# Performance work log

Measured on AMD Instinct MI355X. Metric: run time of the kernel, lower is better.

The kernel has to match this reference:

```python
import jax, jax.numpy as jnp
import numpy as np

N, T, C, H, W = 4, 8, 512, 14, 14
HEADS = 8
D = C // HEADS            # 64 per-head dim
S = T * H * W             # 1568 sequence length
EPS = 1e-8
NEG = -2.0**32 + 1.0      # padding value used by the original module


def setup_inputs() -> dict:
    key = jax.random.key(0)
    ks = jax.random.split(key, 8)
    shp = (N, T, C, H, W)
    scale = 1.0 / np.sqrt(C)
    return {
        "queries": jax.random.normal(ks[0], shp, jnp.float32),
        "keys": jax.random.normal(ks[1], shp, jnp.float32),
        "values": jax.random.normal(ks[2], shp, jnp.float32),
        "Wq": jax.random.normal(ks[3], (C, C), jnp.float32) * scale,
        "bq": jnp.zeros((C,), jnp.float32),
        "Wk": jax.random.normal(ks[4], (C, C), jnp.float32) * scale,
        "bk": jnp.zeros((C,), jnp.float32),
        "Wv": jax.random.normal(ks[5], (C, C), jnp.float32) * scale,
        "bv": jnp.zeros((C,), jnp.float32),
        "gamma": jnp.ones((C,), jnp.float32),
        "beta": jnp.zeros((C,), jnp.float32),
    }


def _proj(x, Wt, b):
    # 1x1 Conv2d + ReLU over channel dim of (N, T, C, H, W)
    y = jnp.einsum('ntchw,oc->ntohw', x, Wt) + b[None, None, :, None, None]
    return jax.nn.relu(y)


def _flatten(x):
    # (N, T, C, H, W) -> (N, T*H*W, C)
    return x.transpose(0, 1, 3, 4, 2).reshape(N, S, C)


def _split_heads(x):
    # torch.cat(torch.chunk(x, HEADS, dim=2), dim=0): (N, S, C) -> (HEADS*N, S, D)
    return x.reshape(N, S, HEADS, D).transpose(2, 0, 1, 3).reshape(HEADS * N, S, D)


def reference(queries, keys, values, Wq, bq, Wk, bk, Wv, bv, gamma, beta):
    Qf = _flatten(_proj(queries, Wq, bq))
    Kf = _flatten(_proj(keys, Wk, bk))
    Vf = _flatten(_proj(values, Wv, bv))
    q_flat = _flatten(queries)   # residual + query mask source
    k_flat = _flatten(keys)      # key mask source

    Q_ = _split_heads(Qf)
    K_ = _split_heads(Kf)
    V_ = _split_heads(Vf)

    scores = jnp.einsum('bqd,bkd->bqk', Q_, K_) / jnp.sqrt(jnp.float32(D))

    # key padding mask: sign(|sum over C|), tiled over heads -> (HEADS*N, 1, S)
    key_mask = jnp.sign(jnp.abs(k_flat.sum(-1)))          # (N, S)
    km = jnp.tile(key_mask, (HEADS, 1))[:, None, :]
    scores = jnp.where(km == 0.0, NEG, scores)

    attn = jax.nn.softmax(scores, axis=-1)

    # query padding mask (multiplicative) -> (HEADS*N, S, 1)
    query_mask = jnp.sign(jnp.abs(q_flat.sum(-1)))        # (N, S)
    qm = jnp.tile(query_mask, (HEADS, 1))[:, :, None]
    attn = attn * qm

    out = jnp.einsum('bqk,bkd->bqd', attn, V_)
    # merge heads back: inverse of _split_heads
    out = out.reshape(HEADS, N, S, D).transpose(1, 2, 0, 3).reshape(N, S, C)

    out = out + q_flat  # residual

    # custom LayerNorm: torch .std() is unbiased (ddof=1)
    mean = out.mean(-1, keepdims=True)
    std = jnp.sqrt(out.var(-1, ddof=1, keepdims=True))
    out = gamma * (out - mean) / (std + EPS) + beta

    # reshape back to (N, T, C, H, W)
    return out.reshape(N, T, H, W, C).transpose(0, 1, 4, 2, 3)
```

## Files before the change

### kernel.cpp

```cpp
#include <hip/hip_runtime.h>
#include <math.h>

#define N_ 4
#define T_ 8
#define C_ 512
#define H_ 14
#define W_ 14
#define HEADS_ 8
#define D_ 64
#define HW_ 196
#define S_ 1568
#define P_TOT 6272
#define NEGL_ (-1.0e38f)
#define EPS_ 1e-8f
#define QSC_ 0.18033688011112042f

typedef __attribute__((ext_vector_type(8))) short short8v;
typedef __attribute__((ext_vector_type(4))) float float4v;
typedef __attribute__((ext_vector_type(4))) unsigned short ushort4v;
typedef unsigned short ushort_t;

__device__ __forceinline__ ushort_t f2bf(float f) {
    union { float f; unsigned u; } a; a.f = f;
    unsigned r = (a.u + 0x7FFFu + ((a.u >> 16) & 1u)) >> 16;
    return (ushort_t)r;
}
__device__ __forceinline__ float bf2f(ushort_t u) {
    union { unsigned u; float f; } t; t.u = ((unsigned)u) << 16; return t.f;
}
__device__ __forceinline__ unsigned cvt_pk_bf16(float lo, float hi) {
    unsigned r;
    asm("v_cvt_pk_bf16_f32 %0, %1, %2" : "=v"(r) : "v"(lo), "v"(hi));
    return r;
}
__device__ __forceinline__ float exp2_fast(float x) {
    float r;
    asm("v_exp_f32 %0, %1" : "=v"(r) : "v"(x));
    return r;
}
__device__ __forceinline__ float max3f(float a, float b, float c) {
    float r;
    asm("v_max3_f32 %0, %1, %2, %3" : "=v"(r) : "v"(a), "v"(b), "v"(c));
    return r;
}
__device__ __forceinline__ float4v mfma16(short8v a, short8v b, float4v c) {
    return __builtin_amdgcn_mfma_f32_16x16x32_bf16(a, b, c, 0, 0, 0);
}
__device__ __forceinline__ void gload_lds16(const void* g, void* l) {
    __builtin_amdgcn_global_load_lds(
        (const __attribute__((address_space(1))) unsigned int*)g,
        (__attribute__((address_space(3))) unsigned int*)l,
        16, 0, 0);
}

__global__ __launch_bounds__(256) void transpose_kernel(
    const float* __restrict__ q_in, const float* __restrict__ k_in,
    const float* __restrict__ v_in, ushort_t* __restrict__ qbf,
    ushort_t* __restrict__ kbf, ushort_t* __restrict__ vbf)
{
    __shared__ float Xs[64][197];
    const int z = blockIdx.z;
    const float* src = (z == 0) ? q_in : (z == 1) ? k_in : v_in;
    ushort_t* dst = (z == 0) ? qbf : (z == 1) ? kbf : vbf;

    const int nt = blockIdx.x;
    const int ct = blockIdx.y;
    const int tid = threadIdx.x;

    const long gbase = ((long)nt * C_ + ct * 64) * HW_;
    #pragma unroll
    for (int i = 0; i < 13; ++i) {
        const int idx = i * 256 + tid;
        if (idx < 3136) {
            const int c = idx / 49;
            const int q4 = idx - c * 49;
            const float4 v = *(const float4*)(src + gbase + c * HW_ + q4 * 4);
            Xs[c][q4 * 4 + 0] = v.x;
            Xs[c][q4 * 4 + 1] = v.y;
            Xs[c][q4 * 4 + 2] = v.z;
            Xs[c][q4 * 4 + 3] = v.w;
        }
    }
    __syncthreads();
    const long pbase = (long)nt * HW_;
    const int c0 = (tid & 15) * 4;
    #pragma unroll
    for (int i = 0; i < 13; ++i) {
        const int idx = i * 256 + tid;
        if (idx < 3136) {
            const int hw = idx >> 4;
            ushort4v pk;
            #pragma unroll
            for (int e = 0; e < 4; ++e) pk[e] = f2bf(Xs[c0 + e][hw]);
            *(ushort4v*)(dst + (pbase + hw) * C_ + ct * 64 + c0) = pk;
        }
    }
}

__global__ __launch_bounds__(256) void wconv_kernel(
    const float* __restrict__ Wq, const float* __restrict__ Wk,
    const float* __restrict__ Wv, ushort_t* __restrict__ Wbf)
{
    const int z = blockIdx.y;
    const float* src = (z == 0) ? Wq : (z == 1) ? Wk : Wv;
    const int q = blockIdx.x * 256 + threadIdx.x;
    const float4 v = *(const float4*)(src + q * 4);
    ushort4v pk;
    pk[0] = f2bf(v.x); pk[1] = f2bf(v.y); pk[2] = f2bf(v.z); pk[3] = f2bf(v.w);
    *(ushort4v*)(Wbf + (long)z * 262144 + q * 4) = pk;
}

__global__ __launch_bounds__(256) void mask_kernel(
    const ushort_t* __restrict__ qbf, const ushort_t* __restrict__ kbf,
    float* __restrict__ qm, float* __restrict__ km)
{
    const int tid = threadIdx.x;
    const int w = tid >> 6, lane = tid & 63;
    const int p = blockIdx.x * 4 + w;
    const short8v qv = *(const short8v*)(qbf + (long)p * C_ + lane * 8);
    const short8v kv = *(const short8v*)(kbf + (long)p * C_ + lane * 8);
    float sq = 0.f, sk = 0.f;
    #pragma unroll
    for (int j = 0; j < 8; ++j) {
        sq += bf2f(((const ushort_t*)&qv)[j]);
        sk += bf2f(((const ushort_t*)&kv)[j]);
    }
    #pragma unroll
    for (int off = 32; off > 0; off >>= 1) {
        sq += __shfl_xor(sq, off, 64);
        sk += __shfl_xor(sk, off, 64);
    }
    if (lane == 0) {
        qm[p] = (sq != 0.f) ? 1.f : 0.f;
        km[p] = (sk != 0.f) ? 0.f : NEGL_;
    }
}

__global__ __launch_bounds__(256) void proj_all(
    const ushort_t* __restrict__ qbf, const ushort_t* __restrict__ kbf,
    const ushort_t* __restrict__ vbf, const ushort_t* __restrict__ Wbf,
    const float* __restrict__ bq, const float* __restrict__ bk,
    const float* __restrict__ bv,
    ushort_t* __restrict__ Qh, ushort_t* __restrict__ Kh,
    ushort_t* __restrict__ Vt)
{
    __shared__ char lds[24576];

    const int fid = blockIdx.x;
    const int xcd = fid & 7;
    const int iin = fid >> 3;
    const int v = xcd * 147 + iin;
    const int z = v / 392;
    const int rem = v - z * 392;
    const int ptile = rem >> 3;
    const int head = rem & 7;

    const ushort_t* Xbf = (z == 0) ? qbf : (z == 1) ? kbf : vbf;
    const ushort_t* Wz = Wbf + (long)z * 262144;
    const float* bias = (z == 0) ? bq : (z == 1) ? bk : bv;
    ushort_t* outp = (z == 0) ? Qh : (z == 1) ? Kh : Vt;
    const bool TR = (z == 2);
    const float osc = (z == 0) ? QSC_ : 1.0f;

    const int tid = threadIdx.x;
    const int w = tid >> 6, lane = tid & 63, lg = lane >> 4, lo = lane & 15;
    const int wr = w >> 1, wc = w & 1;
    const int p0 = ptile * 128;
    const int o0 = head * 64;

    char* Xl = lds;
    char* Wl = lds + 16384;
    const int wbase = (tid & 192) * 16;

    float4v acc[2][4];
    #pragma unroll
    for (int a = 0; a < 2; ++a)
        #pragma unroll
        for (int b = 0; b < 4; ++b) acc[a][b] = (float4v){0.f, 0.f, 0.f, 0.f};

    auto stage = [&](int k0) {
        #pragma unroll
        for (int i = 0; i < 4; ++i) {
            const int sl = tid + i * 256;
            const int row = sl >> 3, sir = sl & 7;
            const int c16 = sir ^ (row & 7);
            gload_lds16(Xbf + (long)(p0 + row) * C_ + k0 + c16 * 8,
                        Xl + i * 4096 + wbase);
        }
        #pragma unroll
        for (int i = 0; i < 2; ++i) {
            const int sl = tid + i * 256;
            const int row = sl >> 3, sir = sl & 7;
            const int c16 = sir ^ (row & 7);
            gload_lds16(Wz + (long)(o0 + row) * C_ + k0 + c16 * 8,
                        Wl + i * 4096 + wbase);
        }
    };

    for (int kstep = 0; kstep < 8; ++kstep) {
        stage(kstep * 64);
        __syncthreads();

        short8v wf[2][2], xf[4][2];
        #pragma unroll
        for (int a = 0; a < 2; ++a) {
            const int row = wc * 32 + a * 16 + lo;
            const int swr = (row & 7) << 4;
            #pragma unroll
            for (int ks = 0; ks < 2; ++ks) {
                const int base = row * 128 + ks * 64 + lg * 8;
                ((uint2*)&wf[a][ks])[0] = *(const uint2*)(Wl + (base ^ swr));
                ((uint2*)&wf[a][ks])[1] = *(const uint2*)(Wl + ((base + 32) ^ swr));
            }
        }
        #pragma unroll
        for (int b = 0; b < 4; ++b) {
            const int row = wr * 64 + b * 16 + lo;
            const int swr = (row & 7) << 4;
            #pragma unroll
            for (int ks = 0; ks < 2; ++ks) {
                const int base = row * 128 + ks * 64 + lg * 8;
                ((uint2*)&xf[b][ks])[0] = *(const uint2*)(Xl + (base ^ swr));
                ((uint2*)&xf[b][ks])[1] = *(const uint2*)(Xl + ((base + 32) ^ swr));
            }
        }
        __builtin_amdgcn_s_setprio(1);
        if (!TR) {
            #pragma unroll
            for (int ks = 0; ks < 2; ++ks)
                #pragma unroll
                for (int a = 0; a < 2; ++a)
                    #pragma unroll
                    for (int b = 0; b < 4; ++b)
                        acc[a][b] = mfma16(wf[a][ks], xf[b][ks], acc[a][b]);
        } else {
            #pragma unroll
            for (int ks = 0; ks < 2; ++ks)
                #pragma unroll
                for (int a = 0; a < 2; ++a)
                    #pragma unroll
                    for (int b = 0; b < 4; ++b)
                        acc[a][b] = mfma16(xf[b][ks], wf[a][ks], acc[a][b]);
        }
        __builtin_amdgcn_s_setprio(0);
        __syncthreads();
    }

    if (!TR) {
        #pragma unroll
        for (int b = 0; b < 4; ++b) {
            const int p = p0 + wr * 64 + b * 16 + lo;
            const int nb = p / S_;
            const int s = p - nb * S_;
            #pragma unroll
            for (int a = 0; a < 2; ++a) {
                const int d0 = wc * 32 + a * 16 + lg * 4;
                const float4v bs = *(const float4v*)(bias + o0 + d0);
                ushort4v pk;
                #pragma unroll
                for (int e = 0; e < 4; ++e) {
                    float vv = acc[a][b][e] + bs[e];
                    vv = vv > 0.f ? vv : 0.f;
                    pk[e] = f2bf(vv * osc);
                }
                *(ushort4v*)(outp + ((long)(head * N_ + nb) * S_ + s) * D_ + d0) = pk;
            }
        }
    } else {
        #pragma unroll
        for (int a = 0; a < 2; ++a) {
            const int d = wc * 32 + a * 16 + lo;
            const float bsc = bias[o0 + d];
            #pragma unroll
            for (int b = 0; b < 4; ++b) {
                const int pb = p0 + wr * 64 + b * 16 + lg * 4;
                const int nb = pb / S_;
                const int s0 = pb - nb * S_;
                ushort4v pk;
                #pragma unroll
                for (int e = 0; e < 4; ++e) {
                    float vv = acc[a][b][e] + bsc;
                    vv = vv > 0.f ? vv : 0.f;
                    pk[e] = f2bf(vv);
                }
                *(ushort4v*)(outp + ((long)(head * N_ + nb) * D_ + d) * S_ + s0) = pk;
            }
        }
    }
}

__global__ __launch_bounds__(256) void attn_kernel(
    const ushort_t* __restrict__ Qh, const ushort_t* __restrict__ Kh,
    const ushort_t* __restrict__ Vt, const float* __restrict__ km,
    ushort_t* __restrict__ Pc, float* __restrict__ Ml)
{
    __shared__ char lds[2 * 16384 + 2 * 256];

    const int tid = threadIdx.x;
    const int lane = tid & 63;
    const int w = tid >> 6;
    const int lg = lane >> 4;
    const int lo = lane & 15;

    const int split = blockIdx.y;
    const int t1 = 7 + split * 6;
    const int t0 = split ? (1 + split * 6) : 0;

    const int fid = blockIdx.x;
    const int x = fid & 7;
    const int j = fid >> 3;
    const int b = x + 8 * (j / 25);
    const int q0 = (j % 25) * 64;
    const int n = b & (N_ - 1);

    const int qrow = q0 + w * 16 + lo;
    const int qcl = qrow < S_ ? qrow : S_ - 1;
    const ushort_t* qp = Qh + ((long)b * S_ + qcl) * D_ + lg * 4;
    short8v qf[2];
    #pragma unroll
    for (int ks = 0; ks < 2; ++ks) {
        ((uint2*)&qf[ks])[0] = *(const uint2*)(qp + ks * 32);
        ((uint2*)&qf[ks])[1] = *(const uint2*)(qp + ks * 32 + 16);
    }

    float4v acc[4];
    #pragma unroll
    for (int dt = 0; dt < 4; ++dt) acc[dt] = (float4v){0.f, 0.f, 0.f, 0.f};
    float m_run = -INFINITY, l_run = 0.f;

    const int sr = tid >> 2;
    const int sseg = tid & 3;
    const int sw = (sr & 7) << 4;
    const int kbase = sr * 128 + sseg * 32;

    uint4 kv0, kv1, vv0, vv1;
    float kmb = 0.f;
    auto issue = [&](int kb) {
        int krow = kb + sr; if (krow >= S_) krow = S_ - 1;
        const uint4* kg = (const uint4*)(Kh + ((long)b * S_ + krow) * D_ + sseg * 16);
        kv0 = kg[0]; kv1 = kg[1];
        int c0 = kb + sseg * 16; if (c0 > S_ - 16) c0 = S_ - 16;
        const uint4* vg = (const uint4*)(Vt + ((long)b * D_ + sr) * S_ + c0);
        vv0 = vg[0]; vv1 = vg[1];
        if (tid < 64) {
            const int kr = kb + tid;
            kmb = (kr < S_) ? km[n * S_ + kr] : NEGL_;
        }
    };
    auto commit = [&](int buf) {
        char* Kl = lds + buf * 16384;
        char* Vl = Kl + 8192;
        float* kmsb = (float*)(lds + 32768 + buf * 256);
        *(uint4*)(Kl + (kbase ^ sw)) = kv0;
        *(uint4*)(Kl + ((kbase + 16) ^ sw)) = kv1;
        *(uint4*)(Vl + (kbase ^ sw)) = vv0;
        *(uint4*)(Vl + ((kbase + 16) ^ sw)) = vv1;
        if (tid < 64) kmsb[tid] = kmb;
    };

    issue(t0 * 64);
    commit(0);
    __syncthreads();
    int cur = 0;

    for (int t = t0; t < t1; ++t) {
        const bool has_next = (t + 1) < t1;
        if (has_next) issue((t + 1) * 64);

        char* Kl = lds + cur * 16384;
        char* Vl = Kl + 8192;
        const float* kmsb = (const float*)(lds + 32768 + cur * 256);

        float4v s[4];
        __builtin_amdgcn_s_setprio(1);
        #pragma unroll
        for (int kt = 0; kt < 4; ++kt) {
            s[kt] = (float4v){0.f, 0.f, 0.f, 0.f};
            #pragma unroll
            for (int ks = 0; ks < 2; ++ks) {
                const int row = kt * 16 + lo;
                const int base = row * 128 + ks * 64 + lg * 8;
                const int swr = (row & 7) << 4;
                short8v kf;
                ((uint2*)&kf)[0] = *(const uint2*)(Kl + (base ^ swr));
                ((uint2*)&kf)[1] = *(const uint2*)(Kl + ((base + 32) ^ swr));
                s[kt] = mfma16(kf, qf[ks], s[kt]);
            }
        }
        __builtin_amdgcn_s_setprio(0);

        float p[4][4];
        #pragma unroll
        for (int kt = 0; kt < 4; ++kt) {
            const float4v bv4 = *(const float4v*)&kmsb[kt * 16 + lg * 4];
            #pragma unroll
            for (int r = 0; r < 4; ++r) p[kt][r] = s[kt][r] + bv4[r];
        }
        const float m1 = max3f(p[0][0], p[0][1], p[0][2]);
        const float m2 = max3f(p[0][3], p[1][0], p[1][1]);
        const float m3 = max3f(p[1][2], p[1][3], p[2][0]);
        const float m4 = max3f(p[2][1], p[2][2], p[2][3]);
        const float m5 = max3f(p[3][0], p[3][1], p[3][2]);
        float mx = max3f(max3f(m1, m2, m3), m4, fmaxf(m5, p[3][3]));
        mx = fmaxf(mx, __shfl_xor(mx, 16, 64));
        mx = fmaxf(mx, __shfl_xor(mx, 32, 64));
        float mn;
        if (__all(mx <= m_run + 8.f)) {
            mn = m_run;
        } else {
            mn = fmaxf(m_run, mx);
            const float alpha = exp2_fast(m_run - mn);
            m_run = mn;
            l_run *= alpha;
            #pragma unroll
            for (int dt = 0; dt < 4; ++dt)
                #pragma unroll
                for (int r = 0; r < 4; ++r) acc[dt][r] *= alpha;
        }
        float rs4[4];
        #pragma unroll
        for (int kt = 0; kt < 4; ++kt) {
            #pragma unroll
            for (int r = 0; r < 4; ++r) p[kt][r] = exp2_fast(p[kt][r] - mn);
            rs4[kt] = (p[kt][0] + p[kt][1]) + (p[kt][2] + p[kt][3]);
        }
        l_run += (rs4[0] + rs4[1]) + (rs4[2] + rs4[3]);

        short8v pf[2];
        #pragma unroll
        for (int kt = 0; kt < 4; ++kt) {
            const unsigned w0 = cvt_pk_bf16(p[kt][0], p[kt][1]);
            const unsigned w1 = cvt_pk_bf16(p[kt][2], p[kt][3]);
            ((unsigned*)&pf[kt >> 1])[(kt & 1) * 2] = w0;
            ((unsigned*)&pf[kt >> 1])[(kt & 1) * 2 + 1] = w1;
        }

        __builtin_amdgcn_s_setprio(1);
        #pragma unroll
        for (int dt = 0; dt < 4; ++dt) {
            #pragma unroll
            for (int ks = 0; ks < 2; ++ks) {
                const int row = dt * 16 + lo;
                const int base = row * 128 + ks * 64 + lg * 8;
                const int swr = (row & 7) << 4;
                short8v vf;
                ((uint2*)&vf)[0] = *(const uint2*)(Vl + (base ^ swr));
                ((uint2*)&vf)[1] = *(const uint2*)(Vl + ((base + 32) ^ swr));
                acc[dt] = mfma16(vf, pf[ks], acc[dt]);
            }
        }
        __builtin_amdgcn_s_setprio(0);

        if (has_next) commit(cur ^ 1);
        __syncthreads();
        cur ^= 1;
    }

    l_run += __shfl_xor(l_run, 16, 64);
    l_run += __shfl_xor(l_run, 32, 64);

    if (qrow < S_) {
        const long rbase = ((long)split * 32 + b) * S_ + qrow;
        if (lg == 0) {
            Ml[rbase * 2] = m_run;
            Ml[rbase * 2 + 1] = l_run;
        }
        ushort_t* P = Pc + rbase * 64;
        #pragma unroll
        for (int dt = 0; dt < 4; ++dt) {
            uint2 uu;
            uu.x = cvt_pk_bf16(acc[dt][0], acc[dt][1]);
            uu.y = cvt_pk_bf16(acc[dt][2], acc[dt][3]);
            *(uint2*)(P + dt * 16 + lg * 4) = uu;
        }
    }
}

__global__ __launch_bounds__(256) void combine_stats_kernel(
    const ushort_t* __restrict__ Pc, const float* __restrict__ Ml,
    const float* __restrict__ qm, const ushort_t* __restrict__ qbf,
    ushort_t* __restrict__ Om, float* __restrict__ stats)
{
    const int tid = threadIdx.x;
    const int wv = tid >> 6, lane = tid & 63;
    const long pos = (long)blockIdx.x * 4 + wv;
    const int n = (int)(pos / S_);
    const int q = (int)(pos - (long)n * S_);
    const int head = lane >> 3;
    const int d0 = (lane & 7) * 8;

    long rb[4];
    float mv[4], lv[4];
    float M = -INFINITY;
    #pragma unroll
    for (int s = 0; s < 4; ++s) {
        rb[s] = ((long)(s * 32 + head * 4 + n) * S_ + q);
        const float2 ml = *(const float2*)(Ml + rb[s] * 2);
        mv[s] = ml.x; lv[s] = ml.y;
        M = fmaxf(M, ml.x);
    }
    float L = 0.f;
    float o[8] = {0.f, 0.f, 0.f, 0.f, 0.f, 0.f, 0.f, 0.f};
    #pragma unroll
    for (int s = 0; s < 4; ++s) {
        const float wgt = exp2_fast(mv[s] - M);
        L = fmaf(lv[s], wgt, L);
        const ushort4v a0 = *(const ushort4v*)(Pc + rb[s] * 64 + d0);
        const ushort4v a1 = *(const ushort4v*)(Pc + rb[s] * 64 + d0 + 4);
        #pragma unroll
        for (int e = 0; e < 4; ++e) {
            o[e] = fmaf(bf2f(a0[e]), wgt, o[e]);
            o[4 + e] = fmaf(bf2f(a1[e]), wgt, o[4 + e]);
        }
    }
    L = fmaxf(L, 1e-20f);
    const float scale = qm[pos] / L;
    const short8v qv = *(const short8v*)(qbf + pos * C_ + lane * 8);
    ushort4v ov0, ov1;
    float sum = 0.f, ssq = 0.f;
    #pragma unroll
    for (int e = 0; e < 8; ++e) {
        const ushort_t ob = f2bf(o[e] * scale);
        if (e < 4) ov0[e] = ob; else ov1[e - 4] = ob;
        const float v = bf2f(ob) + bf2f(((const ushort_t*)&qv)[e]);
        sum += v; ssq += v * v;
    }
    #pragma unroll
    for (int off = 32; off > 0; off >>= 1) {
        sum += __shfl_xor(sum, off, 64);
        ssq += __shfl_xor(ssq, off, 64);
    }
    *(ushort4v*)(Om + pos * C_ + lane * 8) = ov0;
    *(ushort4v*)(Om + pos * C_ + lane * 8 + 4) = ov1;
    if (lane == 0) {
        const float mean = sum * (1.f / 512.f);
        float var = (ssq - sum * mean) * (1.f / 511.f);
        var = var > 0.f ? var : 0.f;
        stats[pos * 2] = mean;
        stats[pos * 2 + 1] = 1.f / (sqrtf(var) + EPS_);
    }
}

__global__ __launch_bounds__(256) void ln_write_kernel(
    const ushort_t* __restrict__ Om, const ushort_t* __restrict__ qbf,
    const float* __restrict__ stats, const float* __restrict__ gamma,
    const float* __restrict__ beta, float* __restrict__ out)
{
    __shared__ float Tl[64][197];
    const int nt = blockIdx.x;
    const int ct = blockIdx.y;
    const int tid = threadIdx.x;

    const int c0 = (tid & 15) * 4;
    float g[4], bb[4];
    #pragma unroll
    for (int e = 0; e < 4; ++e) {
        g[e] = gamma[ct * 64 + c0 + e];
        bb[e] = beta[ct * 64 + c0 + e];
    }

    #pragma unroll
    for (int i = 0; i < 13; ++i) {
        const int idx = i * 256 + tid;
        if (idx < 3136) {
            const int hw = idx >> 4;
            const long p = (long)nt * HW_ + hw;
            const float mean = stats[p * 2];
            const float inv = stats[p * 2 + 1];
            const ushort4v ov = *(const ushort4v*)(Om + p * C_ + ct * 64 + c0);
            const ushort4v qv = *(const ushort4v*)(qbf + p * C_ + ct * 64 + c0);
            #pragma unroll
            for (int e = 0; e < 4; ++e) {
                const float xv = bf2f(ov[e]) + bf2f(qv[e]);
                Tl[c0 + e][hw] = g[e] * (xv - mean) * inv + bb[e];
            }
        }
    }
    __syncthreads();
    const long obase = ((long)nt * C_ + ct * 64) * HW_;
    #pragma unroll
    for (int i = 0; i < 13; ++i) {
        const int idx = i * 256 + tid;
        if (idx < 3136) {
            const int c = idx / 49;
            const int q4 = idx - c * 49;
            float4 v;
            v.x = Tl[c][q4 * 4 + 0];
            v.y = Tl[c][q4 * 4 + 1];
            v.z = Tl[c][q4 * 4 + 2];
            v.w = Tl[c][q4 * 4 + 3];
            *(float4*)(out + obase + c * HW_ + q4 * 4) = v;
        }
    }
}

extern "C" void kernel_launch(void* const* d_in, const int* in_sizes, int n_in,
                              void* d_out, int out_size, void* d_ws, size_t ws_size,
                              hipStream_t stream) {
    const float* q_in  = (const float*)d_in[0];
    const float* k_in  = (const float*)d_in[1];
    const float* v_in  = (const float*)d_in[2];
    const float* Wq    = (const float*)d_in[3];
    const float* bq    = (const float*)d_in[4];
    const float* Wk    = (const float*)d_in[5];
    const float* bk    = (const float*)d_in[6];
    const float* Wv    = (const float*)d_in[7];
    const float* bv    = (const float*)d_in[8];
    const float* gamma = (const float*)d_in[9];
    const float* beta  = (const float*)d_in[10];
    float* out = (float*)d_out;

    const size_t PC = (size_t)P_TOT * C_;
    ushort_t* qbf = (ushort_t*)d_ws;
    ushort_t* kbf = qbf + PC;
    ushort_t* vbf = kbf + PC;
    ushort_t* Wbf = vbf + PC;
    ushort_t* Qh  = Wbf + 3 * (size_t)C_ * C_;
    ushort_t* Kh  = Qh + PC;
    ushort_t* Vt  = Kh + PC;
    ushort_t* Om  = Vt + PC;
    ushort_t* Pc  = Om + PC;
    float* Ml    = (float*)(Pc + 4L * 32 * S_ * 64);
    float* stats = Ml + 4L * 32 * S_ * 2;
    float* qm    = stats + 2 * P_TOT;
    float* km    = qm + P_TOT;

    transpose_kernel<<<dim3(32, 8, 3), 256, 0, stream>>>(q_in, k_in, v_in, qbf, kbf, vbf);
    wconv_kernel<<<dim3(256, 3), 256, 0, stream>>>(Wq, Wk, Wv, Wbf);
    mask_kernel<<<P_TOT / 4, 256, 0, stream>>>(qbf, kbf, qm, km);
    proj_all<<<1176, 256, 0, stream>>>(qbf, kbf, vbf, Wbf, bq, bk, bv, Qh, Kh, Vt);
    attn_kernel<<<dim3(800, 4), 256, 0, stream>>>(Qh, Kh, Vt, km, Pc, Ml);
    combine_stats_kernel<<<P_TOT / 4, 256, 0, stream>>>(Pc, Ml, qm, qbf, Om, stats);
    ln_write_kernel<<<dim3(32, 8), 256, 0, stream>>>(Om, qbf, stats, gamma, beta, out);
}
```

Measured before the change: 105.3 us.

## Stage attention K/V tiles via direct global-to-LDS loads in a single buffer

```diff
diff --git a/kernel.cpp b/kernel.cpp
--- a/kernel.cpp
+++ b/kernel.cpp
@@ -11,6 +11,7 @@
 #define HW_ 196
 #define S_ 1568
 #define P_TOT 6272
+#define KMP_ 1600
 #define NEGL_ (-1.0e38f)
 #define EPS_ 1e-8f
 #define QSC_ 0.18033688011112042f
@@ -51,6 +52,12 @@
         (const __attribute__((address_space(1))) unsigned int*)g,
         (__attribute__((address_space(3))) unsigned int*)l,
         16, 0, 0);
+}
+__device__ __forceinline__ void gload_lds4(const void* g, void* l) {
+    __builtin_amdgcn_global_load_lds(
+        (const __attribute__((address_space(1))) unsigned int*)g,
+        (__attribute__((address_space(3))) unsigned int*)l,
+        4, 0, 0);
 }
 
 __global__ __launch_bounds__(256) void transpose_kernel(
@@ -131,8 +138,14 @@
         sk += __shfl_xor(sk, off, 64);
     }
     if (lane == 0) {
+        const int n = p / S_, s = p - n * S_;
         qm[p] = (sq != 0.f) ? 1.f : 0.f;
-        km[p] = (sk != 0.f) ? 0.f : NEGL_;
+        km[n * KMP_ + s] = (sk != 0.f) ? 0.f : NEGL_;
+    }
+    if (blockIdx.x == 0 && tid < 128) {
+        const int nn = tid >> 5;
+        const int ss = S_ + (tid & 31);
+        km[nn * KMP_ + ss] = NEGL_;
     }
 }
 
@@ -294,7 +307,7 @@
     const ushort_t* __restrict__ Vt, const float* __restrict__ km,
     ushort_t* __restrict__ Pc, float* __restrict__ Ml)
 {
-    __shared__ char lds[2 * 16384 + 2 * 256];
+    __shared__ char lds[16384 + 256];
 
     const int tid = threadIdx.x;
     const int lane = tid & 63;
@@ -313,6 +326,11 @@
     const int q0 = (j % 25) * 64;
     const int n = b & (N_ - 1);
 
+    char* Kl = lds;
+    char* Vl = lds + 8192;
+    const float* kms = (const float*)(lds + 16384);
+    const int wbase = (tid & 192) * 16;
+
     const int qrow = q0 + w * 16 + lo;
     const int qcl = qrow < S_ ? qrow : S_ - 1;
     const ushort_t* qp = Qh + ((long)b * S_ + qcl) * D_ + lg * 4;
@@ -328,48 +346,32 @@
     for (int dt = 0; dt < 4; ++dt) acc[dt] = (float4v){0.f, 0.f, 0.f, 0.f};
     float m_run = -INFINITY, l_run = 0.f;
 
-    const int sr = tid >> 2;
-    const int sseg = tid & 3;
-    const int sw = (sr & 7) << 4;
-    const int kbase = sr * 128 + sseg * 32;
-
-    uint4 kv0, kv1, vv0, vv1;
-    float kmb = 0.f;
-    auto issue = [&](int kb) {
-        int krow = kb + sr; if (krow >= S_) krow = S_ - 1;
-        const uint4* kg = (const uint4*)(Kh + ((long)b * S_ + krow) * D_ + sseg * 16);
-        kv0 = kg[0]; kv1 = kg[1];
-        int c0 = kb + sseg * 16; if (c0 > S_ - 16) c0 = S_ - 16;
-        const uint4* vg = (const uint4*)(Vt + ((long)b * D_ + sr) * S_ + c0);
-        vv0 = vg[0]; vv1 = vg[1];
-        if (tid < 64) {
-            const int kr = kb + tid;
-            kmb = (kr < S_) ? km[n * S_ + kr] : NEGL_;
-        }
+    auto stage = [&](int kb) {
+        #pragma unroll
+        for (int i = 0; i < 2; ++i) {
+            const int s = i * 256 + tid;
+            const int row = s >> 3;
+            const int c16 = (s & 7) ^ (row & 7);
+            int krow = kb + row; if (krow >= S_) krow = S_ - 1;
+            gload_lds16(Kh + ((long)b * S_ + krow) * D_ + c16 * 8,
+                        Kl + i * 4096 + wbase);
+        }
+        #pragma unroll
+        for (int i = 0; i < 2; ++i) {
+            const int s = i * 256 + tid;
+            const int row = s >> 3;
+            const int c16 = (s & 7) ^ (row & 7);
+            int kc = kb + c16 * 8; if (kc > S_ - 8) kc = S_ - 8;
+            gload_lds16(Vt + ((long)b * D_ + row) * S_ + kc,
+                        Vl + i * 4096 + wbase);
+        }
+        if (w == 0)
+            gload_lds4(km + (long)n * KMP_ + kb + lane, (void*)kms);
     };
-    auto commit = [&](int buf) {
-        char* Kl = lds + buf * 16384;
-        char* Vl = Kl + 8192;
-        float* kmsb = (float*)(lds + 32768 + buf * 256);
-        *(uint4*)(Kl + (kbase ^ sw)) = kv0;
-        *(uint4*)(Kl + ((kbase + 16) ^ sw)) = kv1;
-        *(uint4*)(Vl + (kbase ^ sw)) = vv0;
-        *(uint4*)(Vl + ((kbase + 16) ^ sw)) = vv1;
-        if (tid < 64) kmsb[tid] = kmb;
-    };
-
-    issue(t0 * 64);
-    commit(0);
-    __syncthreads();
-    int cur = 0;
 
     for (int t = t0; t < t1; ++t) {
-        const bool has_next = (t + 1) < t1;
-        if (has_next) issue((t + 1) * 64);
-
-        char* Kl = lds + cur * 16384;
-        char* Vl = Kl + 8192;
-        const float* kmsb = (const float*)(lds + 32768 + cur * 256);
+        stage(t * 64);
+        __syncthreads();
 
         float4v s[4];
         __builtin_amdgcn_s_setprio(1);
@@ -392,7 +394,7 @@
         float p[4][4];
         #pragma unroll
         for (int kt = 0; kt < 4; ++kt) {
-            const float4v bv4 = *(const float4v*)&kmsb[kt * 16 + lg * 4];
+            const float4v bv4 = *(const float4v*)&kms[kt * 16 + lg * 4];
             #pragma unroll
             for (int r = 0; r < 4; ++r) p[kt][r] = s[kt][r] + bv4[r];
         }
@@ -450,10 +452,7 @@
             }
         }
         __builtin_amdgcn_s_setprio(0);
-
-        if (has_next) commit(cur ^ 1);
         __syncthreads();
-        cur ^= 1;
     }
 
     l_run += __shfl_xor(l_run, 16, 64);
```

After: 103.7 us. About the same (-1.6%).
